# Kernel tuning notes

Hardware: AMD Instinct MI355X
Metric: run time of the kernel (lower is better)

The kernel has to match this reference:

```python
import jax, jax.numpy as jnp
import numpy as np

N = 50000        # nodes
E = 800000       # random edges (plus N self-loops added in setup)
DIN = 128        # input_dim
H = 128          # hidden_dim
L = 3            # num_layers
EPS = 1e-5       # BatchNorm1d eps


def _bn(x, gamma, beta):
    # BatchNorm1d in training mode: batch stats over node axis, biased variance
    m = x.mean(axis=0)
    v = jnp.mean((x - m) ** 2, axis=0)
    return (x - m) * jax.lax.rsqrt(v + EPS) * gamma + beta


def setup_inputs() -> dict:
    key = jax.random.key(0)
    ks = jax.random.split(key, 11)
    feats = jax.random.normal(ks[0], (N, DIN), dtype=jnp.float32)
    # edge list with self-loops so every node has degree >= 1 (average pooling divides by degree)
    loops = jnp.arange(N, dtype=jnp.int64)
    src = jnp.concatenate([jax.random.randint(ks[1], (E,), 0, N, dtype=jnp.int64), loops])
    dst = jnp.concatenate([jax.random.randint(ks[2], (E,), 0, N, dtype=jnp.int64), loops])
    s = 0.05
    # per-layer MLP params (num_mlp_layers=2: Linear -> BN -> ReLU -> Linear), layer 0 has DIN==H
    W1 = jax.random.normal(ks[3], (L, DIN, H), dtype=jnp.float32) * s
    b1 = jnp.zeros((L, H), jnp.float32)
    g1 = jnp.ones((L, H), jnp.float32)
    be1 = jnp.zeros((L, H), jnp.float32)
    W2 = jax.random.normal(ks[4], (L, H, H), dtype=jnp.float32) * s
    b2 = jnp.zeros((L, H), jnp.float32)
    # outer BatchNorm1d per GNN layer
    og = jnp.ones((L, H), jnp.float32)
    ob = jnp.zeros((L, H), jnp.float32)
    return {"feats": feats, "W1": W1, "b1": b1, "g1": g1, "be1": be1,
            "W2": W2, "b2": b2, "og": og, "ob": ob, "src": src, "dst": dst}


def reference(feats, W1, b1, g1, be1, W2, b2, og, ob, src, dst):
    n = feats.shape[0]
    # degree = spmm(Adj, ones) -- constant across layers
    deg = jax.ops.segment_sum(jnp.ones(src.shape, jnp.float32), dst, num_segments=n)[:, None]
    h = feats
    for l in range(L):
        # pooled = spmm(Adj, h) via edge gather + segment reduce, then 'average' normalize
        pooled = jax.ops.segment_sum(h[src], dst, num_segments=n) / deg
        # GIN-style 2-layer MLP: Linear -> BN -> ReLU -> Linear
        z = jax.nn.relu(_bn(pooled @ W1[l] + b1[l], g1[l], be1[l]))
        z = z @ W2[l] + b2[l]
        # outer BatchNorm + ReLU
        h = jax.nn.relu(_bn(z, og[l], ob[l]))
    return h
```

## Files before the change

### kernel.cpp

```cpp
#include <hip/hip_runtime.h>
#include <hip/hip_bf16.h>
#include <stdint.h>

typedef _Float16 h16;
typedef h16 h16x2 __attribute__((ext_vector_type(2)));
typedef h16 h16x8 __attribute__((ext_vector_type(8)));
typedef float f32x4 __attribute__((ext_vector_type(4)));

#define HF 128
#define EPS 1e-5f
#define BSH 9
#define BROWS 512
#define BCAP 16384
#define ECHUNK 2048
#define SBANKS 8

union pk32 { uint32_t u; h16x2 h; };

static __device__ __forceinline__ uint32_t pack_h16(float a, float b) {
    pk32 c;
    c.h[0] = (h16)a; c.h[1] = (h16)b;
    return c.u;
}

static __device__ __forceinline__ float sum8(const float* __restrict__ st, int idx) {
    float s = 0.f;
#pragma unroll
    for (int b = 0; b < SBANKS; b++) s += st[b * 256 + idx];
    return s;
}

__global__ __launch_bounds__(256) void k_prepscat(const float* __restrict__ W1,
                                                  const float* __restrict__ W2,
                                                  h16* __restrict__ wp,
                                                  const float* __restrict__ feats,
                                                  uint32_t* __restrict__ hbuf, long tot2,
                                                  const int* __restrict__ src,
                                                  const int* __restrict__ dst,
                                                  int* __restrict__ gcursor,
                                                  uint32_t* __restrict__ staging, int ne, int nb,
                                                  int ebk) {
    __shared__ int h[128], gb[128];
    const int bid = (int)blockIdx.x;
    const int tid = threadIdx.x;
    if (bid < ebk) {
        if (tid < nb) h[tid] = 0;
        __syncthreads();
        const int beg = bid * ECHUNK;
        const int end = min(beg + ECHUNK, ne);
        for (int i = beg + tid; i < end; i += 256)
            atomicAdd(&h[dst[i] >> BSH], 1);
        __syncthreads();
        if (tid < nb) {
            int c = h[tid];
            gb[tid] = c ? atomicAdd(&gcursor[tid], c) : 0;
            h[tid] = 0;
        }
        __syncthreads();
        for (int i = beg + tid; i < end; i += 256) {
            int d = dst[i];
            int b = d >> BSH;
            int r = atomicAdd(&h[b], 1);
            staging[(size_t)b * BCAP + gb[b] + r] =
                (uint32_t)src[i] | ((uint32_t)(d & (BROWS - 1)) << 16);
        }
    } else if (bid < ebk + 384) {
        const int wb = bid - ebk;
        const int mat = wb >> 6;
        const int idx = ((wb & 63) << 8) + tid;
        const int l = mat >> 1;
        const float* Wsrc = (mat & 1) ? (W2 + l * 16384) : (W1 + l * 16384);
        const int nn = idx >> 7, k = idx & 127;
        float w = Wsrc[k * 128 + nn];
        int pos = nn * 128 + ((((k >> 3) ^ (nn & 7))) << 3) + (k & 7);
        wp[mat * 16384 + pos] = (h16)w;
    } else {
        long i = (long)(bid - ebk - 384) * 256 + tid;
        if (i < tot2) {
            float2 v = ((const float2*)feats)[i];
            hbuf[i] = pack_h16(v.x, v.y);
        }
    }
}

__global__ __launch_bounds__(256) void k_bbuild(const uint32_t* __restrict__ staging,
                                                const int* __restrict__ gcursor,
                                                int* __restrict__ rowbeg,
                                                int* __restrict__ rowend,
                                                float* __restrict__ deginv,
                                                int* __restrict__ csrsrc, int n) {
    __shared__ int hist[BROWS];
    __shared__ int scan[BROWS];
    const int b = blockIdx.x;
    const int tid = threadIdx.x;
    const int rb = b << BSH;
    const int nrows = min(BROWS, n - rb);
    const int base = b * BCAP;
    const int cnt = gcursor[b];
    hist[tid] = 0; hist[tid + 256] = 0;
    __syncthreads();
    for (int i = tid; i < cnt; i += 256)
        atomicAdd(&hist[staging[base + i] >> 16], 1);
    __syncthreads();
    const int i0 = tid, i1 = tid + 256;
    scan[i0] = hist[i0]; scan[i1] = hist[i1];
    __syncthreads();
    for (int off = 1; off < BROWS; off <<= 1) {
        int v0 = (i0 >= off) ? scan[i0 - off] : 0;
        int v1 = (i1 >= off) ? scan[i1 - off] : 0;
        __syncthreads();
        scan[i0] += v0; scan[i1] += v1;
        __syncthreads();
    }
    for (int r = tid; r < BROWS; r += 256) {
        int c = hist[r];
        int excl = scan[r] - c;
        if (r < nrows) {
            rowbeg[rb + r] = base + excl;
            rowend[rb + r] = base + excl + c;
            deginv[rb + r] = c ? 1.0f / (float)c : 0.f;
        }
        scan[r] = excl;
    }
    __syncthreads();
    for (int i = tid; i < cnt; i += 256) {
        uint32_t e = staging[base + i];
        int pos = atomicAdd(&scan[e >> 16], 1);
        csrsrc[base + pos] = (int)(e & 0xFFFFu);
    }
}

template <int AFF>
__global__ __launch_bounds__(256) void k_spmm(const uint32_t* __restrict__ hp,
                                              const int* __restrict__ rowbeg,
                                              const int* __restrict__ rowend,
                                              const float* __restrict__ deginv,
                                              const float* __restrict__ st,
                                              const float* __restrict__ g,
                                              const float* __restrict__ be,
                                              float inv_n,
                                              const int* __restrict__ csrsrc,
                                              uint32_t* __restrict__ pooled, int n, int np) {
    const int wid  = (int)((blockIdx.x * 256u + threadIdx.x) >> 6);
    const int lane = threadIdx.x & 63;
    if (wid >= np) return;
    const int gg = lane >> 4;
    const int fl = lane & 15;
    uint4* outrow = (uint4*)(pooled + (size_t)wid * 64);
    if (wid >= n) {
        if (gg == 0) outrow[fl] = make_uint4(0u, 0u, 0u, 0u);
        return;
    }

    uint32_t sv[4], cv[4];
    if (AFF) {
        const int c0 = lane * 2, c1 = c0 + 1;
        float m0 = sum8(st, c0) * inv_n, v0 = sum8(st, 128 + c0) * inv_n - m0 * m0;
        float sx = g[c0] * rsqrtf(v0 + EPS), cx = be[c0] - m0 * sx;
        float m1 = sum8(st, c1) * inv_n, v1 = sum8(st, 128 + c1) * inv_n - m1 * m1;
        float sy = g[c1] * rsqrtf(v1 + EPS), cy = be[c1] - m1 * sy;
        uint32_t su = pack_h16(sx, sy);
        uint32_t cu = pack_h16(cx, cy);
#pragma unroll
        for (int w = 0; w < 4; w++) {
            sv[w] = (uint32_t)__shfl((int)su, fl * 4 + w);
            cv[w] = (uint32_t)__shfl((int)cu, fl * 4 + w);
        }
    }

    const h16 z0 = (h16)0.f;
    h16x2 acc[4];
#pragma unroll
    for (int w = 0; w < 4; w++) acc[w] = (h16x2)z0;

    const int beg = rowbeg[wid], end = rowend[wid];
    for (int base = beg; base < end; base += 64) {
        const int rem = end - base;
        const int cnt = rem < 64 ? rem : 64;
        const int off = lane < cnt ? lane : cnt - 1;
        const int idx = csrsrc[base + off];
        for (int j = 0; j < cnt; j += 32) {
            uint4 p[8];
#pragma unroll
            for (int u = 0; u < 8; u++) {
                const int eb = j + u * 4;
                if (eb < cnt) {
                    int ge = eb + gg;
                    int gec = ge < cnt ? ge : cnt - 1;
                    int s = __shfl(idx, gec);
                    p[u] = *(const uint4*)(hp + (size_t)s * 64 + (fl << 2));
                }
            }
#pragma unroll
            for (int u = 0; u < 8; u++) {
                const int eb = j + u * 4;
                if (eb < cnt) {
                    const uint32_t* pw = (const uint32_t*)&p[u];
                    h16x2 v[4];
#pragma unroll
                    for (int w = 0; w < 4; w++) {
                        pk32 t; t.u = pw[w];
                        h16x2 x = t.h;
                        if (AFF) {
                            pk32 s2; s2.u = sv[w];
                            pk32 c2; c2.u = cv[w];
                            x = x * s2.h + c2.h;
                            x[0] = x[0] > z0 ? x[0] : z0;
                            x[1] = x[1] > z0 ? x[1] : z0;
                        }
                        v[w] = x;
                    }
                    if (eb + gg < cnt) {
#pragma unroll
                        for (int w = 0; w < 4; w++) acc[w] = acc[w] + v[w];
                    }
                }
            }
        }
    }

#pragma unroll
    for (int w = 0; w < 4; w++) {
        pk32 t; t.h = acc[w];
        pk32 r1; r1.u = (uint32_t)__shfl_xor((int)t.u, 16);
        t.h = t.h + r1.h;
        pk32 r2; r2.u = (uint32_t)__shfl_xor((int)t.u, 32);
        t.h = t.h + r2.h;
        acc[w] = t.h;
    }

    const float di = deginv[wid];
    uint4 o;
    o.x = pack_h16((float)acc[0][0] * di, (float)acc[0][1] * di);
    o.y = pack_h16((float)acc[1][0] * di, (float)acc[1][1] * di);
    o.z = pack_h16((float)acc[2][0] * di, (float)acc[2][1] * di);
    o.w = pack_h16((float)acc[3][0] * di, (float)acc[3][1] * di);
    if (gg == 0) outrow[fl] = o;
}

template <int MODE>
__global__ __launch_bounds__(256) void k_gemm(const uint32_t* __restrict__ Ap,
                                              const h16* __restrict__ Wp,
                                              const float* __restrict__ bias,
                                              const float* __restrict__ st,
                                              const float* __restrict__ g,
                                              const float* __restrict__ be,
                                              float inv_n,
                                              h16* __restrict__ Y,
                                              float* __restrict__ outstats, int n) {
    __shared__ __align__(16) h16 WT[128 * 128];
    __shared__ float sred[4][128];
    __shared__ float sred2[4][128];
    __shared__ float aff[256];
    const int tid = threadIdx.x;
    const int wave = tid >> 6, lane = tid & 63;

    {
        const char* gsrc = (const char*)Wp + wave * 1024 + lane * 16;
        char* ldst = (char*)&WT[0] + wave * 1024;
#pragma unroll
        for (int i = 0; i < 8; i++) {
            __builtin_amdgcn_global_load_lds(
                (const __attribute__((address_space(1))) uint32_t*)(gsrc + i * 4096),
                (__attribute__((address_space(3))) uint32_t*)(ldst + i * 4096),
                16, 0, 0);
        }
    }
    if (MODE == 1 && tid < 128) {
        float m = sum8(st, tid) * inv_n;
        float v = sum8(st, 128 + tid) * inv_n - m * m;
        float a = g[tid] * rsqrtf(v + EPS);
        aff[tid] = a;
        aff[128 + tid] = be[tid] - m * a;
    }

    const int lrow = lane & 15, quad = lane >> 4;
    const int bx = (int)blockIdx.x * 64;
    const int mb = bx + wave * 16;

    h16x8 ah[4];
    uint4 araw[4];
    {
        const uint32_t* arow = Ap + (size_t)(mb + lrow) * 64 + quad * 4;
#pragma unroll
        for (int kt = 0; kt < 4; kt++)
            araw[kt] = *(const uint4*)(arow + kt * 16);
    }

    __syncthreads();

#pragma unroll
    for (int kt = 0; kt < 4; kt++) {
        if (MODE == 0) {
            ah[kt] = *(const h16x8*)&araw[kt];
        } else {
            const uint32_t* pw = (const uint32_t*)&araw[kt];
            h16x8 t;
#pragma unroll
            for (int j2 = 0; j2 < 4; j2++) {
                pk32 w; w.u = pw[j2];
                int k = kt * 32 + quad * 8 + j2 * 2;
                float x0 = fmaxf(fmaf((float)w.h[0], aff[k],     aff[128 + k]),     0.f);
                float x1 = fmaxf(fmaf((float)w.h[1], aff[k + 1], aff[129 + k]), 0.f);
                t[2 * j2]     = (h16)x0;
                t[2 * j2 + 1] = (h16)x1;
            }
            ah[kt] = t;
        }
    }

    f32x4 acc[8];
#pragma unroll
    for (int nt = 0; nt < 8; nt++) acc[nt] = (f32x4){0.f, 0.f, 0.f, 0.f};

    const int sw = lrow & 7;
#pragma unroll
    for (int nt = 0; nt < 8; nt++) {
        const h16* wbase = &WT[(nt * 16 + lrow) * 128];
#pragma unroll
        for (int kt = 0; kt < 4; kt++) {
            h16x8 bh = *(const h16x8*)(wbase + (((4 * kt + quad) ^ sw) << 3));
            acc[nt] = __builtin_amdgcn_mfma_f32_16x16x32_f16(ah[kt], bh, acc[nt], 0, 0, 0);
        }
    }

#pragma unroll
    for (int nt = 0; nt < 8; nt++) {
        int col = nt * 16 + lrow;
        float bv = bias[col];
        float csum = 0.f, csq = 0.f;
#pragma unroll
        for (int r = 0; r < 4; r++) {
            int row = mb + quad * 4 + r;
            float yv = acc[nt][r] + bv;
            Y[(size_t)row * 128 + col] = (h16)yv;
            if (row < n) { csum += yv; csq += yv * yv; }
        }
        csum += __shfl_xor(csum, 16, 64); csum += __shfl_xor(csum, 32, 64);
        csq  += __shfl_xor(csq,  16, 64); csq  += __shfl_xor(csq,  32, 64);
        if (quad == 0) { sred[wave][col] = csum; sred2[wave][col] = csq; }
    }
    __syncthreads();
    if (tid < 128) {
        float s = sred[0][tid] + sred[1][tid] + sred[2][tid] + sred[3][tid];
        float q = sred2[0][tid] + sred2[1][tid] + sred2[2][tid] + sred2[3][tid];
        const int bank = (int)(blockIdx.x & (SBANKS - 1));
        atomicAdd(&outstats[bank * 256 + tid], s);
        atomicAdd(&outstats[bank * 256 + 128 + tid], q);
    }
}

__global__ __launch_bounds__(256) void k_bnrelu(const uint32_t* __restrict__ Z,
                                                const float* __restrict__ st,
                                                const float* __restrict__ g,
                                                const float* __restrict__ be,
                                                float inv_n,
                                                float* __restrict__ out, long tot4) {
    long i = (long)blockIdx.x * 256 + threadIdx.x;
    if (i >= tot4) return;
    int c = (int)((i * 4) & 127);
    float a[4], cc[4];
#pragma unroll
    for (int j = 0; j < 4; j++) {
        float m = sum8(st, c + j) * inv_n;
        float v = sum8(st, 128 + c + j) * inv_n - m * m;
        a[j] = g[c + j] * rsqrtf(v + EPS);
        cc[j] = be[c + j] - m * a[j];
    }
    uint2 w2 = ((const uint2*)Z)[i];
    pk32 w0; w0.u = w2.x;
    pk32 w1; w1.u = w2.y;
    float4 o;
    o.x = fmaxf(fmaf((float)w0.h[0], a[0], cc[0]), 0.f);
    o.y = fmaxf(fmaf((float)w0.h[1], a[1], cc[1]), 0.f);
    o.z = fmaxf(fmaf((float)w1.h[0], a[2], cc[2]), 0.f);
    o.w = fmaxf(fmaf((float)w1.h[1], a[3], cc[3]), 0.f);
    ((float4*)out)[i] = o;
}

extern "C" void kernel_launch(void* const* d_in, const int* in_sizes, int n_in,
                              void* d_out, int out_size, void* d_ws, size_t ws_size,
                              hipStream_t stream) {
    const float* feats = (const float*)d_in[0];
    const float* W1    = (const float*)d_in[1];
    const float* b1    = (const float*)d_in[2];
    const float* g1    = (const float*)d_in[3];
    const float* be1   = (const float*)d_in[4];
    const float* W2    = (const float*)d_in[5];
    const float* b2    = (const float*)d_in[6];
    const float* og    = (const float*)d_in[7];
    const float* ob    = (const float*)d_in[8];
    const int*   src   = (const int*)d_in[9];
    const int*   dst   = (const int*)d_in[10];

    const int n  = in_sizes[0] / HF;
    const int ne = in_sizes[9];
    const int np = (n + 127) & ~127;
    const int nb = (n + BROWS - 1) >> BSH;

    char* p = (char*)d_ws;
    auto alloc = [&](size_t bytes) -> char* {
        char* r = p;
        p += (bytes + 511) & ~(size_t)511;
        return r;
    };
    uint32_t* hbuf    = (uint32_t*)alloc((size_t)np * 64 * 4);
    uint32_t* pooled  = (uint32_t*)alloc((size_t)np * 64 * 4);
    uint32_t* ybuf    = (uint32_t*)alloc((size_t)np * 64 * 4);
    uint32_t* zb      = (uint32_t*)alloc((size_t)np * 64 * 4);
    h16*      wprep   = (h16*)     alloc(6 * 16384 * 2);
    float*    deginv  = (float*)   alloc((size_t)n * 4);
    int*      rowbeg  = (int*)     alloc((size_t)n * 4);
    int*      rowend  = (int*)     alloc((size_t)n * 4);
    int*      csrsrc  = (int*)     alloc((size_t)nb * BCAP * 4);
    uint32_t* staging = (uint32_t*)alloc((size_t)nb * BCAP * 4);
    char*     zone    = alloc(512 + 6 * SBANKS * 256 * 4);
    int*      gcursor = (int*)zone;
    float*    stats6  = (float*)(zone + 512);

    hipMemsetAsync(zone, 0, 512 + 6 * SBANKS * 256 * 4, stream);

    const long tot2  = (long)n * (HF / 2);
    const long tot4  = tot2 / 2;
    const int bnb    = (int)((tot2 + 255) / 256);
    const int bnb4   = (int)((tot4 + 255) / 256);
    const int spmmb  = np / 4;
    const int gemmb  = np / 64;
    const float inv_n = 1.0f / (float)n;
    const int ebk = (ne + ECHUNK - 1) / ECHUNK;
    const int SL = SBANKS * 256;

    k_prepscat<<<ebk + 384 + bnb, 256, 0, stream>>>(W1, W2, wprep, feats, hbuf, tot2,
                                                    src, dst, gcursor, staging, ne, nb, ebk);
    k_bbuild  <<<nb, 256, 0, stream>>>(staging, gcursor, rowbeg, rowend, deginv, csrsrc, n);

    for (int l = 0; l < 3; l++) {
        float* sY = stats6 + (2 * l) * SL;
        float* sZ = stats6 + (2 * l + 1) * SL;
        if (l == 0)
            k_spmm<0><<<spmmb, 256, 0, stream>>>(hbuf, rowbeg, rowend, deginv,
                                                 nullptr, nullptr, nullptr, inv_n,
                                                 csrsrc, pooled, n, np);
        else
            k_spmm<1><<<spmmb, 256, 0, stream>>>(zb, rowbeg, rowend, deginv,
                                                 stats6 + (2 * (l - 1) + 1) * SL,
                                                 og + (l - 1) * HF, ob + (l - 1) * HF, inv_n,
                                                 csrsrc, pooled, n, np);
        k_gemm<0><<<gemmb, 256, 0, stream>>>(pooled,
                                             wprep + (size_t)(2 * l) * 16384,
                                             b1 + l * HF,
                                             nullptr, nullptr, nullptr, inv_n,
                                             (h16*)ybuf, sY, n);
        k_gemm<1><<<gemmb, 256, 0, stream>>>(ybuf,
                                             wprep + (size_t)(2 * l + 1) * 16384,
                                             b2 + l * HF,
                                             sY, g1 + l * HF, be1 + l * HF, inv_n,
                                             (h16*)zb, sZ, n);
    }
    k_bnrelu<<<bnb4, 256, 0, stream>>>(zb, stats6 + 5 * SL, og + 2 * HF, ob + 2 * HF,
                                       inv_n, (float*)d_out, tot4);
}
```

Measured before the change: 337.4 us.

## Build CSR via global degree atomics and direct scatter instead of bucket staging

Replaces the two-pass bucketed CSR construction (per-bucket staging buffer plus a per-bucket histogram, scan and local scatter) with a global per-node degree count using atomics, a per-bucket scan into rowbeg, and a direct atomic scatter of source indices into csrsrc. This removes the staging buffer and one full read/write pass over the edges. In exchange it adds a kernel launch, 850k global atomics on random addresses for the degree count, and another 850k contended atomics on rowend during the scatter. The neighbour order within each row becomes nondeterministic, which can change floating-point summation order.

```diff
diff --git a/kernel.cpp b/kernel.cpp
--- a/kernel.cpp
+++ b/kernel.cpp
@@ -30,80 +30,51 @@
     return s;
 }
 
-__global__ __launch_bounds__(256) void k_prepscat(const float* __restrict__ W1,
-                                                  const float* __restrict__ W2,
-                                                  h16* __restrict__ wp,
-                                                  const float* __restrict__ feats,
-                                                  uint32_t* __restrict__ hbuf, long tot2,
-                                                  const int* __restrict__ src,
-                                                  const int* __restrict__ dst,
-                                                  int* __restrict__ gcursor,
-                                                  uint32_t* __restrict__ staging, int ne, int nb,
-                                                  int ebk) {
-    __shared__ int h[128], gb[128];
+__global__ __launch_bounds__(256) void k_prep(const float* __restrict__ W1,
+                                              const float* __restrict__ W2,
+                                              h16* __restrict__ wp,
+                                              const float* __restrict__ feats,
+                                              uint32_t* __restrict__ hbuf, long tot2,
+                                              const int* __restrict__ dst,
+                                              int* __restrict__ deg, int ne, int bnb) {
     const int bid = (int)blockIdx.x;
     const int tid = threadIdx.x;
-    if (bid < ebk) {
-        if (tid < nb) h[tid] = 0;
-        __syncthreads();
-        const int beg = bid * ECHUNK;
-        const int end = min(beg + ECHUNK, ne);
-        for (int i = beg + tid; i < end; i += 256)
-            atomicAdd(&h[dst[i] >> BSH], 1);
-        __syncthreads();
-        if (tid < nb) {
-            int c = h[tid];
-            gb[tid] = c ? atomicAdd(&gcursor[tid], c) : 0;
-            h[tid] = 0;
-        }
-        __syncthreads();
-        for (int i = beg + tid; i < end; i += 256) {
-            int d = dst[i];
-            int b = d >> BSH;
-            int r = atomicAdd(&h[b], 1);
-            staging[(size_t)b * BCAP + gb[b] + r] =
-                (uint32_t)src[i] | ((uint32_t)(d & (BROWS - 1)) << 16);
-        }
-    } else if (bid < ebk + 384) {
-        const int wb = bid - ebk;
-        const int mat = wb >> 6;
-        const int idx = ((wb & 63) << 8) + tid;
+    if (bid < 384) {
+        const int mat = bid >> 6;
+        const int idx = ((bid & 63) << 8) + tid;
         const int l = mat >> 1;
         const float* Wsrc = (mat & 1) ? (W2 + l * 16384) : (W1 + l * 16384);
         const int nn = idx >> 7, k = idx & 127;
         float w = Wsrc[k * 128 + nn];
         int pos = nn * 128 + ((((k >> 3) ^ (nn & 7))) << 3) + (k & 7);
         wp[mat * 16384 + pos] = (h16)w;
-    } else {
-        long i = (long)(bid - ebk - 384) * 256 + tid;
+    } else if (bid < 384 + bnb) {
+        long i = (long)(bid - 384) * 256 + tid;
         if (i < tot2) {
             float2 v = ((const float2*)feats)[i];
             hbuf[i] = pack_h16(v.x, v.y);
         }
-    }
-}
-
-__global__ __launch_bounds__(256) void k_bbuild(const uint32_t* __restrict__ staging,
-                                                const int* __restrict__ gcursor,
-                                                int* __restrict__ rowbeg,
-                                                int* __restrict__ rowend,
-                                                float* __restrict__ deginv,
-                                                int* __restrict__ csrsrc, int n) {
-    __shared__ int hist[BROWS];
+    } else {
+        const int beg = (bid - 384 - bnb) * ECHUNK;
+        const int end = min(beg + ECHUNK, ne);
+        for (int i = beg + tid; i < end; i += 256)
+            atomicAdd(&deg[dst[i]], 1);
+    }
+}
+
+__global__ __launch_bounds__(256) void k_rowscan(const int* __restrict__ deg,
+                                                 int* __restrict__ rowbeg,
+                                                 int* __restrict__ rowend,
+                                                 float* __restrict__ deginv, int n) {
     __shared__ int scan[BROWS];
     const int b = blockIdx.x;
     const int tid = threadIdx.x;
     const int rb = b << BSH;
-    const int nrows = min(BROWS, n - rb);
     const int base = b * BCAP;
-    const int cnt = gcursor[b];
-    hist[tid] = 0; hist[tid + 256] = 0;
-    __syncthreads();
-    for (int i = tid; i < cnt; i += 256)
-        atomicAdd(&hist[staging[base + i] >> 16], 1);
-    __syncthreads();
     const int i0 = tid, i1 = tid + 256;
-    scan[i0] = hist[i0]; scan[i1] = hist[i1];
+    const int d0 = (rb + i0) < n ? deg[rb + i0] : 0;
+    const int d1 = (rb + i1) < n ? deg[rb + i1] : 0;
+    scan[i0] = d0; scan[i1] = d1;
     __syncthreads();
     for (int off = 1; off < BROWS; off <<= 1) {
         int v0 = (i0 >= off) ? scan[i0 - off] : 0;
@@ -112,21 +83,30 @@
         scan[i0] += v0; scan[i1] += v1;
         __syncthreads();
     }
-    for (int r = tid; r < BROWS; r += 256) {
-        int c = hist[r];
-        int excl = scan[r] - c;
-        if (r < nrows) {
-            rowbeg[rb + r] = base + excl;
-            rowend[rb + r] = base + excl + c;
-            deginv[rb + r] = c ? 1.0f / (float)c : 0.f;
-        }
-        scan[r] = excl;
-    }
-    __syncthreads();
-    for (int i = tid; i < cnt; i += 256) {
-        uint32_t e = staging[base + i];
-        int pos = atomicAdd(&scan[e >> 16], 1);
-        csrsrc[base + pos] = (int)(e & 0xFFFFu);
+    if (rb + i0 < n) {
+        int excl = scan[i0] - d0;
+        rowbeg[rb + i0] = base + excl;
+        rowend[rb + i0] = base + excl;
+        deginv[rb + i0] = d0 ? 1.0f / (float)d0 : 0.f;
+    }
+    if (rb + i1 < n) {
+        int excl = scan[i1] - d1;
+        rowbeg[rb + i1] = base + excl;
+        rowend[rb + i1] = base + excl;
+        deginv[rb + i1] = d1 ? 1.0f / (float)d1 : 0.f;
+    }
+}
+
+__global__ __launch_bounds__(256) void k_scatter(const int* __restrict__ src,
+                                                 const int* __restrict__ dst,
+                                                 int* __restrict__ rowend,
+                                                 int* __restrict__ csrsrc, int ne) {
+    const int beg = (int)blockIdx.x * ECHUNK;
+    const int end = min(beg + ECHUNK, ne);
+    for (int i = beg + threadIdx.x; i < end; i += 256) {
+        int r = dst[i];
+        int pos = atomicAdd(&rowend[r], 1);
+        csrsrc[pos] = src[i];
     }
 }
 
@@ -413,12 +393,12 @@
     int*      rowbeg  = (int*)     alloc((size_t)n * 4);
     int*      rowend  = (int*)     alloc((size_t)n * 4);
     int*      csrsrc  = (int*)     alloc((size_t)nb * BCAP * 4);
-    uint32_t* staging = (uint32_t*)alloc((size_t)nb * BCAP * 4);
-    char*     zone    = alloc(512 + 6 * SBANKS * 256 * 4);
-    int*      gcursor = (int*)zone;
-    float*    stats6  = (float*)(zone + 512);
-
-    hipMemsetAsync(zone, 0, 512 + 6 * SBANKS * 256 * 4, stream);
+    const size_t degb = ((size_t)n * 4 + 511) & ~(size_t)511;
+    char*     zone    = alloc(degb + 6 * SBANKS * 256 * 4);
+    int*      deg     = (int*)zone;
+    float*    stats6  = (float*)(zone + degb);
+
+    hipMemsetAsync(zone, 0, degb + 6 * SBANKS * 256 * 4, stream);
 
     const long tot2  = (long)n * (HF / 2);
     const long tot4  = tot2 / 2;
@@ -430,9 +410,10 @@
     const int ebk = (ne + ECHUNK - 1) / ECHUNK;
     const int SL = SBANKS * 256;
 
-    k_prepscat<<<ebk + 384 + bnb, 256, 0, stream>>>(W1, W2, wprep, feats, hbuf, tot2,
-                                                    src, dst, gcursor, staging, ne, nb, ebk);
-    k_bbuild  <<<nb, 256, 0, stream>>>(staging, gcursor, rowbeg, rowend, deginv, csrsrc, n);
+    k_prep   <<<384 + bnb + ebk, 256, 0, stream>>>(W1, W2, wprep, feats, hbuf, tot2,
+                                                   dst, deg, ne, bnb);
+    k_rowscan<<<nb, 256, 0, stream>>>(deg, rowbeg, rowend, deginv, n);
+    k_scatter<<<ebk, 256, 0, stream>>>(src, dst, rowend, csrsrc, ne);
 
     for (int l = 0; l < 3; l++) {
         float* sY = stats6 + (2 * l) * SL;
```

Result: slower. 405.3 us (+20.1%).
